# Optimization experiments

Measured on AMD Instinct MI355X. Metric: run time of the kernel, lower is better.

Reference implementation:

```python
import jax, jax.numpy as jnp
import numpy as np
import math

NUM_HEADS = 16
HEAD_SIZE = 64
HIDDEN = NUM_HEADS * HEAD_SIZE
LN_EPS = 1e-12


def setup_inputs() -> dict:
    key = jax.random.key(0)
    ks = jax.random.split(key, 8)
    B, Lw, Le, H = 8, 512, 64, HIDDEN
    scale = 0.02
    return {
        "word_hidden_states": jax.random.normal(ks[0], (B, Lw, H), jnp.float32),
        "entity_hidden_states": jax.random.normal(ks[1], (B, Le, H), jnp.float32),
        "attention_mask": jnp.zeros((B, 1, 1, Lw + Le), jnp.float32),
        "Wq": jax.random.normal(ks[2], (H, H), jnp.float32) * scale,
        "bq": jnp.zeros((H,), jnp.float32),
        "Wk": jax.random.normal(ks[3], (H, H), jnp.float32) * scale,
        "bk": jnp.zeros((H,), jnp.float32),
        "Wv": jax.random.normal(ks[4], (H, H), jnp.float32) * scale,
        "bv": jnp.zeros((H,), jnp.float32),
        "Wo": jax.random.normal(ks[5], (H, H), jnp.float32) * scale,
        "bo": jnp.zeros((H,), jnp.float32),
        "ln_w": jnp.ones((H,), jnp.float32),
        "ln_b": jnp.zeros((H,), jnp.float32),
    }


def _layernorm(x, w, b):
    u = jnp.mean(x, axis=-1, keepdims=True)
    s = jnp.mean(jnp.square(x - u), axis=-1, keepdims=True)
    return w * ((x - u) / jnp.sqrt(s + LN_EPS)) + b


def reference(word_hidden_states, entity_hidden_states, attention_mask,
              Wq, bq, Wk, bk, Wv, bv, Wo, bo, ln_w, ln_b):
    B, Lw, H = word_hidden_states.shape
    x = jnp.concatenate([word_hidden_states, entity_hidden_states], axis=1)  # [B,S,H]
    S = x.shape[1]

    def heads(t):  # [B,S,H] -> [B,nh,S,hd]
        return t.reshape(B, S, NUM_HEADS, HEAD_SIZE).transpose(0, 2, 1, 3)

    q = heads(x @ Wq + bq)
    k = heads(x @ Wk + bk)
    v = heads(x @ Wv + bv)

    scores = jnp.einsum("bhqd,bhkd->bhqk", q, k) / math.sqrt(HEAD_SIZE)
    scores = scores + attention_mask  # additive mask, broadcast [B,1,1,S]
    probs = jax.nn.softmax(scores, axis=-1)
    ctx = jnp.einsum("bhqk,bhkd->bhqd", probs, v)
    ctx = ctx.transpose(0, 2, 1, 3).reshape(B, S, H)

    # SelfOutput (shared weights) applied per-stream; equivalent on concat since
    # residual is the concatenated input and LayerNorm is per-token.
    out = _layernorm(ctx @ Wo + bo + x, ln_w, ln_b)
    return out[:, :Lw, :], out[:, Lw:, :]
```

## Files before the change

### kernel.cpp

```cpp
#include <hip/hip_runtime.h>

#define NHEADS 16
#define HDIM   64
#define HID    1024
#define BATCH  8
#define LW     512
#define LE     64
#define SEQ    576
#define MTOT   (BATCH * SEQ)

typedef unsigned short u16;
typedef __bf16 bf16x8 __attribute__((ext_vector_type(8)));
typedef float  f32x4  __attribute__((ext_vector_type(4)));

__device__ __forceinline__ u16 f2bf(float f) {
  union { float f; unsigned int i; } x;
  x.f = f;
  unsigned int u = x.i;
  unsigned int r = (u + 0x7FFFu + ((u >> 16) & 1u)) >> 16;
  return (u16)r;
}
__device__ __forceinline__ unsigned int pk2(float a, float b) {
  return (unsigned int)f2bf(a) | ((unsigned int)f2bf(b) << 16);
}

__device__ __forceinline__ void gload16(const u16* g, u16* l) {
  __builtin_amdgcn_global_load_lds(
      (const __attribute__((address_space(1))) void*)g,
      (__attribute__((address_space(3))) void*)l, 16, 0, 0);
}

__global__ __launch_bounds__(256) void prep_k(
    const float* __restrict__ w0, const float* __restrict__ w1,
    const float* __restrict__ w2, const float* __restrict__ w3,
    u16* __restrict__ wt,
    const float* __restrict__ word, const float* __restrict__ ent,
    u16* __restrict__ xb)
{
  const int bid = blockIdx.x, tid = threadIdx.x;
  if (bid < 4096) {
    __shared__ u16 tile[32][33];
    const int z = bid >> 10, rem = bid & 1023;
    const int bx = rem & 31, by = rem >> 5;
    const float* src = (z == 0) ? w0 : (z == 1) ? w1 : (z == 2) ? w2 : w3;
    u16* dst = wt + (size_t)z * HID * HID;
    const int tx = tid & 31, ty = tid >> 5;
    const int nx = bx * 32, ky = by * 32;
#pragma unroll
    for (int j = 0; j < 4; ++j)
      tile[ty * 4 + j][tx] = f2bf(src[(size_t)(ky + ty * 4 + j) * HID + nx + tx]);
    __syncthreads();
#pragma unroll
    for (int j = 0; j < 4; ++j)
      dst[(size_t)(nx + ty * 4 + j) * HID + ky + tx] = tile[tx][ty * 4 + j];
  } else {
    const int row = bid - 4096;
    const int bb = row / SEQ, ss = row - bb * SEQ;
    const float* src = (ss < LW) ? word + (size_t)(bb * LW + ss) * HID
                                 : ent  + (size_t)(bb * LE + (ss - LW)) * HID;
    float4 v = *(const float4*)(src + tid * 4);
    ushort4 o;
    o.x = f2bf(v.x); o.y = f2bf(v.y); o.z = f2bf(v.z); o.w = f2bf(v.w);
    *(ushort4*)(xb + (size_t)row * HID + tid * 4) = o;
  }
}

__global__ __launch_bounds__(256) void qkv_gemm_k(
    const u16* __restrict__ xb, const u16* __restrict__ wt,
    const float* __restrict__ bq, const float* __restrict__ bk, const float* __restrict__ bv,
    u16* __restrict__ q_ws, u16* __restrict__ k_ws, u16* __restrict__ v_ws)
{
  __shared__ u16 sh[4 * 64 * 68];
  const int which = blockIdx.z;
  const u16* W = wt + (size_t)which * HID * HID;
  const float* bias = (which == 0) ? bq : (which == 1) ? bk : bv;
  const int m0 = blockIdx.x * 128, n0 = blockIdx.y * 128;
  const int tid = threadIdx.x, lane = tid & 63, wv = tid >> 6;
  const int lr = lane & 15, quad = lane >> 4;
  const int wm = (wv >> 1) * 64, wn = (wv & 1) * 64;

  const int subrow = lane >> 3;
  const int gsw = ((lane & 7) ^ subrow) * 8;
  const int fsw = lr & 7;

  u16* As = sh;
  u16* Bs = sh + 8192;

  const f32x4 fz = {0.f, 0.f, 0.f, 0.f};
  f32x4 acc[4][4];
#pragma unroll
  for (int a = 0; a < 4; ++a)
#pragma unroll
    for (int b = 0; b < 4; ++b) acc[a][b] = fz;

  for (int ki = 0; ki < 16; ++ki) {
    const int k0 = ki * 64;
#pragma unroll
    for (int j = 0; j < 4; ++j) {
      int row = (wv * 4 + j) * 8 + subrow;
      u16* ldst = sh + ((wv * 4 + j) * 64 + lane) * 8;
      gload16(xb + (size_t)(m0 + row) * HID + k0 + gsw, ldst);
      gload16(W  + (size_t)(n0 + row) * HID + k0 + gsw, ldst + 8192);
    }
    __syncthreads();
#pragma unroll
    for (int ks = 0; ks < 2; ++ks) {
      bf16x8 af[4], bfr[4];
#pragma unroll
      for (int i = 0; i < 4; ++i) {
        af[i]  = *(const bf16x8*)(&As[(wm + i * 16 + lr) * 64 + (((ks * 4 + quad) ^ fsw) * 8)]);
        bfr[i] = *(const bf16x8*)(&Bs[(wn + i * 16 + lr) * 64 + (((ks * 4 + quad) ^ fsw) * 8)]);
      }
      if (which < 2) {
#pragma unroll
        for (int a = 0; a < 4; ++a)
#pragma unroll
          for (int b = 0; b < 4; ++b)
            acc[a][b] = __builtin_amdgcn_mfma_f32_16x16x32_bf16(bfr[a], af[b], acc[a][b], 0, 0, 0);
      } else {
#pragma unroll
        for (int a = 0; a < 4; ++a)
#pragma unroll
          for (int b = 0; b < 4; ++b)
            acc[a][b] = __builtin_amdgcn_mfma_f32_16x16x32_bf16(af[a], bfr[b], acc[a][b], 0, 0, 0);
      }
    }
    __syncthreads();
  }

  u16* tb = sh + wv * (64 * 68);
  const int head = (n0 + wn) >> 6;
  const int mbase = m0 + wm;
  const int bb = mbase / SEQ;
  const int ssb = mbase - bb * SEQ;

  if (which < 2) {
    float4 bias4[4];
#pragma unroll
    for (int ni = 0; ni < 4; ++ni)
      bias4[ni] = *(const float4*)(bias + n0 + wn + ni * 16 + quad * 4);
#pragma unroll
    for (int mi = 0; mi < 4; ++mi)
#pragma unroll
      for (int ni = 0; ni < 4; ++ni) {
        uint2 w2v;
        w2v.x = pk2(acc[ni][mi][0] + bias4[ni].x, acc[ni][mi][1] + bias4[ni].y);
        w2v.y = pk2(acc[ni][mi][2] + bias4[ni].z, acc[ni][mi][3] + bias4[ni].w);
        *(uint2*)(&tb[(mi * 16 + lr) * 68 + ni * 16 + quad * 4]) = w2v;
      }
    u16* drow = (which == 0 ? q_ws : k_ws)
              + ((size_t)(bb * NHEADS + head) * SEQ + ssb) * HDIM;
#pragma unroll
    for (int i = 0; i < 8; ++i) {
      int rrow = i * 8 + (lane >> 3);
      int seg = lane & 7;
      bf16x8 v8 = *(const bf16x8*)(&tb[rrow * 68 + seg * 8]);
      *(bf16x8*)(drow + (size_t)rrow * HDIM + seg * 8) = v8;
    }
  } else {
    float bcol[4];
#pragma unroll
    for (int ni = 0; ni < 4; ++ni) bcol[ni] = bias[n0 + wn + ni * 16 + lr];
#pragma unroll
    for (int mi = 0; mi < 4; ++mi)
#pragma unroll
      for (int ni = 0; ni < 4; ++ni) {
        uint2 w2v;
        w2v.x = pk2(acc[mi][ni][0] + bcol[ni], acc[mi][ni][1] + bcol[ni]);
        w2v.y = pk2(acc[mi][ni][2] + bcol[ni], acc[mi][ni][3] + bcol[ni]);
        *(uint2*)(&tb[(ni * 16 + lr) * 68 + (mi >> 1) * 32 + quad * 8 + (mi & 1) * 4]) = w2v;
      }
    u16* dcol = v_ws + ((size_t)(bb * NHEADS + head) * HDIM) * SEQ + ssb;
#pragma unroll
    for (int i = 0; i < 8; ++i) {
      int d = i * 8 + (lane >> 3);
      int seg = lane & 7;
      bf16x8 v8 = *(const bf16x8*)(&tb[d * 68 + seg * 8]);
      *(bf16x8*)(dcol + (size_t)d * SEQ + seg * 8) = v8;
    }
  }
}

__global__ __launch_bounds__(256) void attn_k(
    const u16* __restrict__ q_ws, const u16* __restrict__ k_ws,
    const u16* __restrict__ v_ws, const float* __restrict__ mask,
    u16* __restrict__ ctxh)
{
  __shared__ u16 Ks[4096];
  __shared__ u16 Vs[4096];
  __shared__ float ms[576];
  const int bhx = blockIdx.x, qt = blockIdx.y;
  const int b = bhx >> 4, h = bhx & 15;
  const int tid = threadIdx.x, lane = tid & 63, wv = tid >> 6;
  const int lr = lane & 15, quad = lane >> 4;
  const int q0 = qt * 64 + wv * 16;
  const u16* kbh = k_ws + (size_t)bhx * SEQ * HDIM;
  const u16* vbh = v_ws + (size_t)bhx * HDIM * SEQ;
  const u16* qp  = q_ws + ((size_t)bhx * SEQ + q0) * HDIM;
  const float* mrow = mask + b * SEQ;

  if (tid < 144) *(float4*)(&ms[tid * 4]) = *(const float4*)(mrow + tid * 4);

  const int subrow = lane >> 3;
  const int gsw = (lane & 7) ^ subrow;

  bf16x8 qf[2];
  qf[0] = *(const bf16x8*)(qp + lr * HDIM + quad * 8);
  qf[1] = *(const bf16x8*)(qp + lr * HDIM + 32 + quad * 8);

  const f32x4 fz = {0.f, 0.f, 0.f, 0.f};
  f32x4 oa[4] = {fz, fz, fz, fz};
  f32x4 rsv = fz;
  const int fA = lr & 7;

  for (int ci = 0; ci < 9; ++ci) {
    const int c = ci * 64;
#pragma unroll
    for (int j = 0; j < 2; ++j) {
      int row = (wv * 2 + j) * 8 + subrow;
      gload16(kbh + ((size_t)(c + row)) * HDIM + gsw * 8,
              &Ks[((wv * 2 + j) * 64 + lane) * 8]);
      gload16(vbh + (size_t)row * SEQ + c + gsw * 8,
              &Vs[((wv * 2 + j) * 64 + lane) * 8]);
    }
    __syncthreads();
    f32x4 s[4] = {fz, fz, fz, fz};
#pragma unroll
    for (int ks = 0; ks < 2; ++ks)
#pragma unroll
      for (int t = 0; t < 4; ++t) {
        bf16x8 kf = *(const bf16x8*)(&Ks[(t * 16 + lr) * 64 + (((ks * 4 + quad) ^ fA) * 8)]);
        s[t] = __builtin_amdgcn_mfma_f32_16x16x32_bf16(kf, qf[ks], s[t], 0, 0, 0);
      }
    unsigned int pk0[4], pk1[4];
#pragma unroll
    for (int t = 0; t < 4; ++t) {
      float4 mv = *(const float4*)(&ms[c + t * 16 + quad * 4]);
      s[t][0] = __expf(s[t][0] * 0.125f + mv.x);
      s[t][1] = __expf(s[t][1] * 0.125f + mv.y);
      s[t][2] = __expf(s[t][2] * 0.125f + mv.z);
      s[t][3] = __expf(s[t][3] * 0.125f + mv.w);
      rsv += s[t];
      pk0[t] = pk2(s[t][0], s[t][1]);
      pk1[t] = pk2(s[t][2], s[t][3]);
    }
#pragma unroll
    for (int ks = 0; ks < 2; ++ks) {
      union { unsigned int u[4]; bf16x8 v; } ap;
      ap.u[0] = pk0[ks * 2];     ap.u[1] = pk1[ks * 2];
      ap.u[2] = pk0[ks * 2 + 1]; ap.u[3] = pk1[ks * 2 + 1];
#pragma unroll
      for (int n = 0; n < 4; ++n) {
        bf16x8 vf = *(const bf16x8*)(&Vs[(n * 16 + lr) * 64 + (((ks * 4 + quad) ^ fA) * 8)]);
        oa[n] = __builtin_amdgcn_mfma_f32_16x16x32_bf16(ap.v, vf, oa[n], 0, 0, 0);
      }
    }
    __syncthreads();
  }

  float rl = rsv[0] + rsv[1] + rsv[2] + rsv[3];
  rl += __shfl_xor(rl, 16);
  rl += __shfl_xor(rl, 32);
  float inv = 1.0f / rl;
  float invr[4];
#pragma unroll
  for (int r = 0; r < 4; ++r) invr[r] = __shfl(inv, quad * 4 + r);

  u16* pw = (wv < 2) ? &Ks[wv * 2048] : &Vs[(wv - 2) * 2048];
#pragma unroll
  for (int n = 0; n < 4; ++n)
#pragma unroll
    for (int r = 0; r < 4; ++r)
      pw[(quad * 4 + r) * 68 + n * 16 + lr] = f2bf(oa[n][r] * invr[r]);
  const int token0 = b * SEQ + q0;
  u16* cb = ctxh + ((size_t)h * MTOT + token0) * HDIM;
#pragma unroll
  for (int i = 0; i < 2; ++i) {
    int row = lane & 15;
    int seg = (lane >> 4) + i * 4;
    bf16x8 v8 = *(const bf16x8*)(&pw[row * 68 + seg * 8]);
    *(bf16x8*)(cb + (size_t)row * HDIM + seg * 8) = v8;
  }
}

__global__ __launch_bounds__(256) void out_gemm_k(
    const u16* __restrict__ ctxh, const u16* __restrict__ wto,
    const float* __restrict__ bo,
    const float* __restrict__ word, const float* __restrict__ ent,
    float* __restrict__ y)
{
  __shared__ u16 sh[10240];
  u16* As = sh;
  u16* Bs = sh + 2048;
  const int m0 = blockIdx.x * 32, n0 = blockIdx.y * 128;
  const int tid = threadIdx.x, lane = tid & 63, wv = tid >> 6;
  const int lr = lane & 15, quad = lane >> 4;
  const int wn = wv * 32;
  const int subrow = lane >> 3;
  const int gsw = ((lane & 7) ^ subrow) * 8;
  const int fsw = lr & 7;

  const f32x4 fz = {0.f, 0.f, 0.f, 0.f};
  f32x4 acc[2][2];
#pragma unroll
  for (int mi = 0; mi < 2; ++mi)
#pragma unroll
    for (int ni = 0; ni < 2; ++ni) acc[mi][ni] = fz;

  for (int hb = 0; hb < 16; ++hb) {
    {
      int row = wv * 8 + subrow;
      gload16(ctxh + ((size_t)hb * MTOT + (m0 + row)) * HDIM + gsw,
              As + (wv * 64 + lane) * 8);
    }
#pragma unroll
    for (int j = 0; j < 4; ++j) {
      int row = (wv * 4 + j) * 8 + subrow;
      gload16(wto + (size_t)(n0 + row) * HID + hb * 64 + gsw,
              Bs + ((wv * 4 + j) * 64 + lane) * 8);
    }
    __syncthreads();
#pragma unroll
    for (int ks = 0; ks < 2; ++ks) {
      const int kc = (((ks * 4 + quad) ^ fsw) * 8);
      bf16x8 af[2], bfr[2];
#pragma unroll
      for (int i = 0; i < 2; ++i) {
        af[i]  = *(const bf16x8*)(&As[(i * 16 + lr) * 64 + kc]);
        bfr[i] = *(const bf16x8*)(&Bs[(wn + i * 16 + lr) * 64 + kc]);
      }
#pragma unroll
      for (int mi = 0; mi < 2; ++mi)
#pragma unroll
        for (int ni = 0; ni < 2; ++ni)
          acc[mi][ni] = __builtin_amdgcn_mfma_f32_16x16x32_bf16(af[mi], bfr[ni], acc[mi][ni], 0, 0, 0);
    }
    __syncthreads();
  }

#pragma unroll
  for (int mi = 0; mi < 2; ++mi) {
    int rowb = m0 + mi * 16 + quad * 4;
#pragma unroll
    for (int r = 0; r < 4; ++r) {
      int row = rowb + r;
      int bb = row / SEQ, ss = row - bb * SEQ;
      const float* res = (ss < LW) ? (word + (size_t)(bb * LW + ss) * HID)
                                   : (ent  + (size_t)(bb * LE + (ss - LW)) * HID);
#pragma unroll
      for (int ni = 0; ni < 2; ++ni) {
        int col = n0 + wn + ni * 16 + lr;
        y[(size_t)row * HID + col] = acc[mi][ni][r] + bo[col] + res[col];
      }
    }
  }
}

__global__ __launch_bounds__(256) void ln_k(
    const float* __restrict__ y, const float* __restrict__ lnw,
    const float* __restrict__ lnb, float* __restrict__ out)
{
  const int row = blockIdx.x;
  const int tid = threadIdx.x;
  __shared__ float ssum[4], sqq[4];

  const float* yr = y + (size_t)row * HID;
  float4 v = *(const float4*)(yr + tid * 4);
  float s = v.x + v.y + v.z + v.w;
  float q = v.x * v.x + v.y * v.y + v.z * v.z + v.w * v.w;
#pragma unroll
  for (int o = 32; o > 0; o >>= 1) { s += __shfl_xor(s, o); q += __shfl_xor(q, o); }
  if ((tid & 63) == 0) { ssum[tid >> 6] = s; sqq[tid >> 6] = q; }
  __syncthreads();
  s = ssum[0] + ssum[1] + ssum[2] + ssum[3];
  q = sqq[0] + sqq[1] + sqq[2] + sqq[3];
  float mean = s * (1.0f / HID);
  float var  = q * (1.0f / HID) - mean * mean;
  float rstd = rsqrtf(var + 1e-12f);

  int bb = row / SEQ, ss2 = row - bb * SEQ;
  float* dst = (ss2 < LW)
             ? out + (size_t)(bb * LW + ss2) * HID
             : out + (size_t)BATCH * LW * HID + (size_t)(bb * LE + (ss2 - LW)) * HID;

  float4 w4 = *(const float4*)(lnw + tid * 4);
  float4 b4 = *(const float4*)(lnb + tid * 4);
  float4 o4;
  o4.x = w4.x * (v.x - mean) * rstd + b4.x;
  o4.y = w4.y * (v.y - mean) * rstd + b4.y;
  o4.z = w4.z * (v.z - mean) * rstd + b4.z;
  o4.w = w4.w * (v.w - mean) * rstd + b4.w;
  *(float4*)(dst + tid * 4) = o4;
}

extern "C" void kernel_launch(void* const* d_in, const int* in_sizes, int n_in,
                              void* d_out, int out_size, void* d_ws, size_t ws_size,
                              hipStream_t stream) {
  const float* word = (const float*)d_in[0];
  const float* ent  = (const float*)d_in[1];
  const float* mask = (const float*)d_in[2];
  const float* Wq   = (const float*)d_in[3];
  const float* bq   = (const float*)d_in[4];
  const float* Wk   = (const float*)d_in[5];
  const float* bk   = (const float*)d_in[6];
  const float* Wv   = (const float*)d_in[7];
  const float* bv   = (const float*)d_in[8];
  const float* Wo   = (const float*)d_in[9];
  const float* bo   = (const float*)d_in[10];
  const float* lnw  = (const float*)d_in[11];
  const float* lnb  = (const float*)d_in[12];

  char* base = (char*)d_ws;
  u16*   wt   = (u16*)base;
  u16*   q_ws = (u16*)(base + (size_t)8 * 1024 * 1024);
  u16*   k_ws = q_ws + (size_t)MTOT * HID;
  u16*   v_ws = k_ws + (size_t)MTOT * HID;
  u16*   ctxh = v_ws + (size_t)MTOT * HID;
  char*  xy   = (char*)(ctxh + (size_t)MTOT * HID);
  u16*   xb   = (u16*)xy;
  float* y    = (float*)xy;

  hipLaunchKernelGGL(prep_k, dim3(4096 + MTOT), dim3(256), 0, stream,
                     Wq, Wk, Wv, Wo, wt, word, ent, xb);
  hipLaunchKernelGGL(qkv_gemm_k, dim3(MTOT / 128, HID / 128, 3), dim3(256), 0, stream,
                     xb, wt, bq, bk, bv, q_ws, k_ws, v_ws);
  hipLaunchKernelGGL(attn_k, dim3(BATCH * NHEADS, SEQ / 64), dim3(256), 0, stream,
                     q_ws, k_ws, v_ws, mask, ctxh);
  hipLaunchKernelGGL(out_gemm_k, dim3(MTOT / 32, HID / 128), dim3(256), 0, stream,
                     ctxh, wt + (size_t)3 * HID * HID, bo, word, ent, y);
  hipLaunchKernelGGL(ln_k, dim3(MTOT), dim3(256), 0, stream,
                     y, lnw, lnb, (float*)d_out);
}
```

Baseline: 197.2 us.

## Rewrite QKV GEMM as 256x256 tile, 8-wave, double-buffered pipelined kernel

```diff
diff --git a/kernel.cpp b/kernel.cpp
--- a/kernel.cpp
+++ b/kernel.cpp
@@ -65,118 +65,263 @@
   }
 }
 
-__global__ __launch_bounds__(256) void qkv_gemm_k(
+__device__ __forceinline__ void qkv_kstep(
+    u16* sh, const u16* asrc, const u16* bsrc, const int s, const int bo,
+    const bool g1, const bool g2, const bool vlast, const int which,
+    const int wm, const int wn, const int lr, const int quad, const int fsw,
+    const int tid, f32x4 (&acc)[8][4])
+{
+  u16* As = sh + bo;
+  u16* Bs = sh + bo + 16384;
+  const int obo = 32768 - bo;
+  bf16x8 afa[4][2], afb[4][2], bfr[4][2];
+
+#pragma unroll
+  for (int mi = 0; mi < 4; ++mi)
+#pragma unroll
+    for (int ks = 0; ks < 2; ++ks)
+      afa[mi][ks] = *(const bf16x8*)(&As[(wm + mi * 16 + lr) * 64 + (((ks * 4 + quad) ^ fsw) * 8)]);
+#pragma unroll
+  for (int ni = 0; ni < 2; ++ni)
+#pragma unroll
+    for (int ks = 0; ks < 2; ++ks)
+      bfr[ni][ks] = *(const bf16x8*)(&Bs[(wn + ni * 16 + lr) * 64 + (((ks * 4 + quad) ^ fsw) * 8)]);
+  if (g1) {
+    gload16(bsrc + (size_t)2 * 64 * HID + (s + 1) * 64, sh + obo + 16384 + 2 * 4096 + tid * 8);
+    gload16(bsrc + (size_t)3 * 64 * HID + (s + 1) * 64, sh + obo + 16384 + 3 * 4096 + tid * 8);
+  }
+  asm volatile("s_waitcnt lgkmcnt(8)" ::: "memory");
+  __builtin_amdgcn_s_barrier();
+  asm volatile("s_waitcnt lgkmcnt(0)" ::: "memory");
+  __builtin_amdgcn_sched_barrier(0);
+  __builtin_amdgcn_s_setprio(1);
+  if (which < 2) {
+#pragma unroll
+    for (int mi = 0; mi < 4; ++mi)
+#pragma unroll
+      for (int ni = 0; ni < 2; ++ni)
+#pragma unroll
+        for (int ks = 0; ks < 2; ++ks)
+          acc[mi][ni] = __builtin_amdgcn_mfma_f32_16x16x32_bf16(bfr[ni][ks], afa[mi][ks], acc[mi][ni], 0, 0, 0);
+  } else {
+#pragma unroll
+    for (int mi = 0; mi < 4; ++mi)
+#pragma unroll
+      for (int ni = 0; ni < 2; ++ni)
+#pragma unroll
+        for (int ks = 0; ks < 2; ++ks)
+          acc[mi][ni] = __builtin_amdgcn_mfma_f32_16x16x32_bf16(afa[mi][ks], bfr[ni][ks], acc[mi][ni], 0, 0, 0);
+  }
+  __builtin_amdgcn_s_setprio(0);
+  __builtin_amdgcn_s_barrier();
+
+#pragma unroll
+  for (int ni = 2; ni < 4; ++ni)
+#pragma unroll
+    for (int ks = 0; ks < 2; ++ks)
+      bfr[ni][ks] = *(const bf16x8*)(&Bs[(wn + ni * 16 + lr) * 64 + (((ks * 4 + quad) ^ fsw) * 8)]);
+  if (g2) {
+    gload16(asrc + (size_t)0 * 64 * HID + (s + 2) * 64, sh + bo + 0 * 4096 + tid * 8);
+    gload16(asrc + (size_t)2 * 64 * HID + (s + 2) * 64, sh + bo + 2 * 4096 + tid * 8);
+  }
+  __builtin_amdgcn_s_barrier();
+  asm volatile("s_waitcnt lgkmcnt(0)" ::: "memory");
+  __builtin_amdgcn_sched_barrier(0);
+  __builtin_amdgcn_s_setprio(1);
+  if (which < 2) {
+#pragma unroll
+    for (int mi = 0; mi < 4; ++mi)
+#pragma unroll
+      for (int ni = 2; ni < 4; ++ni)
+#pragma unroll
+        for (int ks = 0; ks < 2; ++ks)
+          acc[mi][ni] = __builtin_amdgcn_mfma_f32_16x16x32_bf16(bfr[ni][ks], afa[mi][ks], acc[mi][ni], 0, 0, 0);
+  } else {
+#pragma unroll
+    for (int mi = 0; mi < 4; ++mi)
+#pragma unroll
+      for (int ni = 2; ni < 4; ++ni)
+#pragma unroll
+        for (int ks = 0; ks < 2; ++ks)
+          acc[mi][ni] = __builtin_amdgcn_mfma_f32_16x16x32_bf16(afa[mi][ks], bfr[ni][ks], acc[mi][ni], 0, 0, 0);
+  }
+  __builtin_amdgcn_s_setprio(0);
+  __builtin_amdgcn_s_barrier();
+
+#pragma unroll
+  for (int mi = 0; mi < 4; ++mi)
+#pragma unroll
+    for (int ks = 0; ks < 2; ++ks)
+      afb[mi][ks] = *(const bf16x8*)(&As[(wm + 64 + mi * 16 + lr) * 64 + (((ks * 4 + quad) ^ fsw) * 8)]);
+  if (g2) {
+    gload16(bsrc + (size_t)0 * 64 * HID + (s + 2) * 64, sh + bo + 16384 + 0 * 4096 + tid * 8);
+    gload16(bsrc + (size_t)1 * 64 * HID + (s + 2) * 64, sh + bo + 16384 + 1 * 4096 + tid * 8);
+  }
+  __builtin_amdgcn_s_barrier();
+  asm volatile("s_waitcnt lgkmcnt(0)" ::: "memory");
+  __builtin_amdgcn_sched_barrier(0);
+  __builtin_amdgcn_s_setprio(1);
+  if (which < 2) {
+#pragma unroll
+    for (int mi = 0; mi < 4; ++mi)
+#pragma unroll
+      for (int ni = 0; ni < 2; ++ni)
+#pragma unroll
+        for (int ks = 0; ks < 2; ++ks)
+          acc[4 + mi][ni] = __builtin_amdgcn_mfma_f32_16x16x32_bf16(bfr[ni][ks], afb[mi][ks], acc[4 + mi][ni], 0, 0, 0);
+  } else {
+#pragma unroll
+    for (int mi = 0; mi < 4; ++mi)
+#pragma unroll
+      for (int ni = 0; ni < 2; ++ni)
+#pragma unroll
+        for (int ks = 0; ks < 2; ++ks)
+          acc[4 + mi][ni] = __builtin_amdgcn_mfma_f32_16x16x32_bf16(afb[mi][ks], bfr[ni][ks], acc[4 + mi][ni], 0, 0, 0);
+  }
+  __builtin_amdgcn_s_setprio(0);
+  __builtin_amdgcn_s_barrier();
+
+  if (g2) {
+    gload16(asrc + (size_t)1 * 64 * HID + (s + 2) * 64, sh + bo + 1 * 4096 + tid * 8);
+    gload16(asrc + (size_t)3 * 64 * HID + (s + 2) * 64, sh + bo + 3 * 4096 + tid * 8);
+  }
+  __builtin_amdgcn_s_barrier();
+  __builtin_amdgcn_sched_barrier(0);
+  __builtin_amdgcn_s_setprio(1);
+  if (which < 2) {
+#pragma unroll
+    for (int mi = 0; mi < 4; ++mi)
+#pragma unroll
+      for (int ni = 2; ni < 4; ++ni)
+#pragma unroll
+        for (int ks = 0; ks < 2; ++ks)
+          acc[4 + mi][ni] = __builtin_amdgcn_mfma_f32_16x16x32_bf16(bfr[ni][ks], afb[mi][ks], acc[4 + mi][ni], 0, 0, 0);
+  } else {
+#pragma unroll
+    for (int mi = 0; mi < 4; ++mi)
+#pragma unroll
+      for (int ni = 2; ni < 4; ++ni)
+#pragma unroll
+        for (int ks = 0; ks < 2; ++ks)
+          acc[4 + mi][ni] = __builtin_amdgcn_mfma_f32_16x16x32_bf16(afb[mi][ks], bfr[ni][ks], acc[4 + mi][ni], 0, 0, 0);
+  }
+  __builtin_amdgcn_s_setprio(0);
+  if (!vlast) asm volatile("s_waitcnt vmcnt(6)" ::: "memory");
+  else        asm volatile("s_waitcnt vmcnt(0)" ::: "memory");
+  __builtin_amdgcn_s_barrier();
+}
+
+__global__ __launch_bounds__(512, 2) void qkv_gemm_k(
     const u16* __restrict__ xb, const u16* __restrict__ wt,
     const float* __restrict__ bq, const float* __restrict__ bk, const float* __restrict__ bv,
     u16* __restrict__ q_ws, u16* __restrict__ k_ws, u16* __restrict__ v_ws)
 {
-  __shared__ u16 sh[4 * 64 * 68];
+  __shared__ u16 sh[65536];
   const int which = blockIdx.z;
   const u16* W = wt + (size_t)which * HID * HID;
   const float* bias = (which == 0) ? bq : (which == 1) ? bk : bv;
-  const int m0 = blockIdx.x * 128, n0 = blockIdx.y * 128;
+  const int m0 = blockIdx.x * 256, n0 = blockIdx.y * 256;
   const int tid = threadIdx.x, lane = tid & 63, wv = tid >> 6;
   const int lr = lane & 15, quad = lane >> 4;
-  const int wm = (wv >> 1) * 64, wn = (wv & 1) * 64;
-
-  const int subrow = lane >> 3;
-  const int gsw = ((lane & 7) ^ subrow) * 8;
+  const int wm = (wv >> 2) * 128, wn = (wv & 3) * 64;
   const int fsw = lr & 7;
 
-  u16* As = sh;
-  u16* Bs = sh + 8192;
+  const int srow = tid >> 3;
+  const int goff = ((tid & 7) ^ (srow & 7)) * 8;
+  const u16* asrc = xb + (size_t)(m0 + srow) * HID + goff;
+  const u16* bsrc = W  + (size_t)(n0 + srow) * HID + goff;
+
+  gload16(asrc + (size_t)0 * 64 * HID, sh + 0 * 4096 + tid * 8);
+  gload16(asrc + (size_t)1 * 64 * HID, sh + 1 * 4096 + tid * 8);
+  gload16(asrc + (size_t)2 * 64 * HID, sh + 2 * 4096 + tid * 8);
+  gload16(asrc + (size_t)3 * 64 * HID, sh + 3 * 4096 + tid * 8);
+  gload16(bsrc + (size_t)0 * 64 * HID, sh + 16384 + 0 * 4096 + tid * 8);
+  gload16(bsrc + (size_t)1 * 64 * HID, sh + 16384 + 1 * 4096 + tid * 8);
+  gload16(bsrc + (size_t)2 * 64 * HID, sh + 16384 + 2 * 4096 + tid * 8);
+  gload16(bsrc + (size_t)3 * 64 * HID, sh + 16384 + 3 * 4096 + tid * 8);
+  gload16(asrc + (size_t)0 * 64 * HID + 64, sh + 32768 + 0 * 4096 + tid * 8);
+  gload16(asrc + (size_t)2 * 64 * HID + 64, sh + 32768 + 2 * 4096 + tid * 8);
+  gload16(bsrc + (size_t)0 * 64 * HID + 64, sh + 32768 + 16384 + 0 * 4096 + tid * 8);
+  gload16(bsrc + (size_t)1 * 64 * HID + 64, sh + 32768 + 16384 + 1 * 4096 + tid * 8);
+  gload16(asrc + (size_t)1 * 64 * HID + 64, sh + 32768 + 1 * 4096 + tid * 8);
+  gload16(asrc + (size_t)3 * 64 * HID + 64, sh + 32768 + 3 * 4096 + tid * 8);
+  asm volatile("s_waitcnt vmcnt(6)" ::: "memory");
+  __builtin_amdgcn_s_barrier();
 
   const f32x4 fz = {0.f, 0.f, 0.f, 0.f};
-  f32x4 acc[4][4];
-#pragma unroll
-  for (int a = 0; a < 4; ++a)
+  f32x4 acc[8][4];
+#pragma unroll
+  for (int a = 0; a < 8; ++a)
 #pragma unroll
     for (int b = 0; b < 4; ++b) acc[a][b] = fz;
 
-  for (int ki = 0; ki < 16; ++ki) {
-    const int k0 = ki * 64;
-#pragma unroll
-    for (int j = 0; j < 4; ++j) {
-      int row = (wv * 4 + j) * 8 + subrow;
-      u16* ldst = sh + ((wv * 4 + j) * 64 + lane) * 8;
-      gload16(xb + (size_t)(m0 + row) * HID + k0 + gsw, ldst);
-      gload16(W  + (size_t)(n0 + row) * HID + k0 + gsw, ldst + 8192);
-    }
-    __syncthreads();
-#pragma unroll
-    for (int ks = 0; ks < 2; ++ks) {
-      bf16x8 af[4], bfr[4];
-#pragma unroll
-      for (int i = 0; i < 4; ++i) {
-        af[i]  = *(const bf16x8*)(&As[(wm + i * 16 + lr) * 64 + (((ks * 4 + quad) ^ fsw) * 8)]);
-        bfr[i] = *(const bf16x8*)(&Bs[(wn + i * 16 + lr) * 64 + (((ks * 4 + quad) ^ fsw) * 8)]);
-      }
-      if (which < 2) {
-#pragma unroll
-        for (int a = 0; a < 4; ++a)
-#pragma unroll
-          for (int b = 0; b < 4; ++b)
-            acc[a][b] = __builtin_amdgcn_mfma_f32_16x16x32_bf16(bfr[a], af[b], acc[a][b], 0, 0, 0);
-      } else {
-#pragma unroll
-        for (int a = 0; a < 4; ++a)
-#pragma unroll
-          for (int b = 0; b < 4; ++b)
-            acc[a][b] = __builtin_amdgcn_mfma_f32_16x16x32_bf16(af[a], bfr[b], acc[a][b], 0, 0, 0);
-      }
-    }
-    __syncthreads();
+  for (int s = 0; s < 16; s += 2) {
+    qkv_kstep(sh, asrc, bsrc, s,     0,     true,   s < 14, s >= 14, which,
+              wm, wn, lr, quad, fsw, tid, acc);
+    qkv_kstep(sh, asrc, bsrc, s + 1, 32768, s < 14, s < 13, s >= 13, which,
+              wm, wn, lr, quad, fsw, tid, acc);
   }
 
   u16* tb = sh + wv * (64 * 68);
   const int head = (n0 + wn) >> 6;
-  const int mbase = m0 + wm;
-  const int bb = mbase / SEQ;
-  const int ssb = mbase - bb * SEQ;
 
   if (which < 2) {
     float4 bias4[4];
 #pragma unroll
     for (int ni = 0; ni < 4; ++ni)
       bias4[ni] = *(const float4*)(bias + n0 + wn + ni * 16 + quad * 4);
-#pragma unroll
-    for (int mi = 0; mi < 4; ++mi)
-#pragma unroll
-      for (int ni = 0; ni < 4; ++ni) {
-        uint2 w2v;
-        w2v.x = pk2(acc[ni][mi][0] + bias4[ni].x, acc[ni][mi][1] + bias4[ni].y);
-        w2v.y = pk2(acc[ni][mi][2] + bias4[ni].z, acc[ni][mi][3] + bias4[ni].w);
-        *(uint2*)(&tb[(mi * 16 + lr) * 68 + ni * 16 + quad * 4]) = w2v;
+    u16* qk = (which == 0 ? q_ws : k_ws);
+#pragma unroll
+    for (int g = 0; g < 2; ++g) {
+      const int mbase = m0 + wm + g * 64;
+      const int bb = mbase / SEQ;
+      const int ssb = mbase - bb * SEQ;
+#pragma unroll
+      for (int mi = 0; mi < 4; ++mi)
+#pragma unroll
+        for (int ni = 0; ni < 4; ++ni) {
+          const f32x4 a = acc[g * 4 + mi][ni];
+          uint2 w2v;
+          w2v.x = pk2(a[0] + bias4[ni].x, a[1] + bias4[ni].y);
+          w2v.y = pk2(a[2] + bias4[ni].z, a[3] + bias4[ni].w);
+          *(uint2*)(&tb[(mi * 16 + lr) * 68 + ni * 16 + quad * 4]) = w2v;
+        }
+      u16* drow = qk + ((size_t)(bb * NHEADS + head) * SEQ + ssb) * HDIM;
+#pragma unroll
+      for (int i = 0; i < 8; ++i) {
+        int rrow = i * 8 + (lane >> 3);
+        int seg = lane & 7;
+        bf16x8 v8 = *(const bf16x8*)(&tb[rrow * 68 + seg * 8]);
+        *(bf16x8*)(drow + (size_t)rrow * HDIM + seg * 8) = v8;
       }
-    u16* drow = (which == 0 ? q_ws : k_ws)
-              + ((size_t)(bb * NHEADS + head) * SEQ + ssb) * HDIM;
-#pragma unroll
-    for (int i = 0; i < 8; ++i) {
-      int rrow = i * 8 + (lane >> 3);
-      int seg = lane & 7;
-      bf16x8 v8 = *(const bf16x8*)(&tb[rrow * 68 + seg * 8]);
-      *(bf16x8*)(drow + (size_t)rrow * HDIM + seg * 8) = v8;
     }
   } else {
     float bcol[4];
 #pragma unroll
     for (int ni = 0; ni < 4; ++ni) bcol[ni] = bias[n0 + wn + ni * 16 + lr];
 #pragma unroll
-    for (int mi = 0; mi < 4; ++mi)
-#pragma unroll
-      for (int ni = 0; ni < 4; ++ni) {
-        uint2 w2v;
-        w2v.x = pk2(acc[mi][ni][0] + bcol[ni], acc[mi][ni][1] + bcol[ni]);
-        w2v.y = pk2(acc[mi][ni][2] + bcol[ni], acc[mi][ni][3] + bcol[ni]);
-        *(uint2*)(&tb[(ni * 16 + lr) * 68 + (mi >> 1) * 32 + quad * 8 + (mi & 1) * 4]) = w2v;
+    for (int g = 0; g < 2; ++g) {
+      const int mbase = m0 + wm + g * 64;
+      const int bb = mbase / SEQ;
+      const int ssb = mbase - bb * SEQ;
+#pragma unroll
+      for (int mi = 0; mi < 4; ++mi)
+#pragma unroll
+        for (int ni = 0; ni < 4; ++ni) {
+          const f32x4 a = acc[g * 4 + mi][ni];
+          uint2 w2v;
+          w2v.x = pk2(a[0] + bcol[ni], a[1] + bcol[ni]);
+          w2v.y = pk2(a[2] + bcol[ni], a[3] + bcol[ni]);
+          *(uint2*)(&tb[(ni * 16 + lr) * 68 + (mi >> 1) * 32 + quad * 8 + (mi & 1) * 4]) = w2v;
+        }
+      u16* dcol = v_ws + ((size_t)(bb * NHEADS + head) * HDIM) * SEQ + ssb;
+#pragma unroll
+      for (int i = 0; i < 8; ++i) {
+        int d = i * 8 + (lane >> 3);
+        int seg = lane & 7;
+        bf16x8 v8 = *(const bf16x8*)(&tb[d * 68 + seg * 8]);
+        *(bf16x8*)(dcol + (size_t)d * SEQ + seg * 8) = v8;
       }
-    u16* dcol = v_ws + ((size_t)(bb * NHEADS + head) * HDIM) * SEQ + ssb;
-#pragma unroll
-    for (int i = 0; i < 8; ++i) {
-      int d = i * 8 + (lane >> 3);
-      int seg = lane & 7;
-      bf16x8 v8 = *(const bf16x8*)(&tb[d * 68 + seg * 8]);
-      *(bf16x8*)(dcol + (size_t)d * SEQ + seg * 8) = v8;
     }
   }
 }
@@ -422,7 +567,7 @@
 
   hipLaunchKernelGGL(prep_k, dim3(4096 + MTOT), dim3(256), 0, stream,
                      Wq, Wk, Wv, Wo, wt, word, ent, xb);
-  hipLaunchKernelGGL(qkv_gemm_k, dim3(MTOT / 128, HID / 128, 3), dim3(256), 0, stream,
+  hipLaunchKernelGGL(qkv_gemm_k, dim3(MTOT / 256, HID / 256, 3), dim3(512), 0, stream,
                      xb, wt, bq, bk, bv, q_ws, k_ws, v_ws);
   hipLaunchKernelGGL(attn_k, dim3(BATCH * NHEADS, SEQ / 64), dim3(256), 0, stream,
                      q_ws, k_ws, v_ws, mask, ctxh);
```

Result: slower. 232.3 us (+17.8%).

## Double-buffer QKV GEMM with 256x128 tiles, 8 waves, and split-phase prefetch

Applied to the files above, without the earlier changes.

```diff
diff --git a/kernel.cpp b/kernel.cpp
--- a/kernel.cpp
+++ b/kernel.cpp
@@ -65,26 +65,39 @@
   }
 }
 
-__global__ __launch_bounds__(256) void qkv_gemm_k(
+__global__ __launch_bounds__(512, 2) void qkv_gemm_k(
     const u16* __restrict__ xb, const u16* __restrict__ wt,
     const float* __restrict__ bq, const float* __restrict__ bk, const float* __restrict__ bv,
     u16* __restrict__ q_ws, u16* __restrict__ k_ws, u16* __restrict__ v_ws)
 {
-  __shared__ u16 sh[4 * 64 * 68];
+  __shared__ u16 sh[49152];
   const int which = blockIdx.z;
   const u16* W = wt + (size_t)which * HID * HID;
   const float* bias = (which == 0) ? bq : (which == 1) ? bk : bv;
-  const int m0 = blockIdx.x * 128, n0 = blockIdx.y * 128;
+  const int m0 = blockIdx.x * 256, n0 = blockIdx.y * 128;
   const int tid = threadIdx.x, lane = tid & 63, wv = tid >> 6;
   const int lr = lane & 15, quad = lane >> 4;
   const int wm = (wv >> 1) * 64, wn = (wv & 1) * 64;
-
-  const int subrow = lane >> 3;
-  const int gsw = ((lane & 7) ^ subrow) * 8;
   const int fsw = lr & 7;
 
-  u16* As = sh;
-  u16* Bs = sh + 8192;
+  const int srow = tid >> 3;
+  const int goff = ((tid & 7) ^ (srow & 7)) * 8;
+  const u16* asrc = xb + (size_t)(m0 + srow) * HID + goff;
+  const u16* bsrc = W  + (size_t)(n0 + srow) * HID + goff;
+  const int ldst = tid * 8;
+
+  gload16(asrc + (size_t)0 * 64 * HID, sh + 0 * 4096 + ldst);
+  gload16(asrc + (size_t)1 * 64 * HID, sh + 1 * 4096 + ldst);
+  gload16(asrc + (size_t)2 * 64 * HID, sh + 2 * 4096 + ldst);
+  gload16(asrc + (size_t)3 * 64 * HID, sh + 3 * 4096 + ldst);
+  gload16(bsrc + (size_t)0 * 64 * HID, sh + 16384 + 0 * 4096 + ldst);
+  gload16(bsrc + (size_t)1 * 64 * HID, sh + 16384 + 1 * 4096 + ldst);
+  gload16(asrc + (size_t)0 * 64 * HID + 64, sh + 24576 + 0 * 4096 + ldst);
+  gload16(asrc + (size_t)1 * 64 * HID + 64, sh + 24576 + 1 * 4096 + ldst);
+  gload16(asrc + (size_t)2 * 64 * HID + 64, sh + 24576 + 2 * 4096 + ldst);
+  gload16(asrc + (size_t)3 * 64 * HID + 64, sh + 24576 + 3 * 4096 + ldst);
+  asm volatile("s_waitcnt vmcnt(4)" ::: "memory");
+  __builtin_amdgcn_s_barrier();
 
   const f32x4 fz = {0.f, 0.f, 0.f, 0.f};
   f32x4 acc[4][4];
@@ -93,39 +106,88 @@
 #pragma unroll
     for (int b = 0; b < 4; ++b) acc[a][b] = fz;
 
-  for (int ki = 0; ki < 16; ++ki) {
-    const int k0 = ki * 64;
-#pragma unroll
-    for (int j = 0; j < 4; ++j) {
-      int row = (wv * 4 + j) * 8 + subrow;
-      u16* ldst = sh + ((wv * 4 + j) * 64 + lane) * 8;
-      gload16(xb + (size_t)(m0 + row) * HID + k0 + gsw, ldst);
-      gload16(W  + (size_t)(n0 + row) * HID + k0 + gsw, ldst + 8192);
-    }
-    __syncthreads();
-#pragma unroll
-    for (int ks = 0; ks < 2; ++ks) {
-      bf16x8 af[4], bfr[4];
-#pragma unroll
-      for (int i = 0; i < 4; ++i) {
-        af[i]  = *(const bf16x8*)(&As[(wm + i * 16 + lr) * 64 + (((ks * 4 + quad) ^ fsw) * 8)]);
-        bfr[i] = *(const bf16x8*)(&Bs[(wn + i * 16 + lr) * 64 + (((ks * 4 + quad) ^ fsw) * 8)]);
-      }
-      if (which < 2) {
-#pragma unroll
-        for (int a = 0; a < 4; ++a)
-#pragma unroll
-          for (int b = 0; b < 4; ++b)
-            acc[a][b] = __builtin_amdgcn_mfma_f32_16x16x32_bf16(bfr[a], af[b], acc[a][b], 0, 0, 0);
-      } else {
-#pragma unroll
-        for (int a = 0; a < 4; ++a)
-#pragma unroll
-          for (int b = 0; b < 4; ++b)
-            acc[a][b] = __builtin_amdgcn_mfma_f32_16x16x32_bf16(af[a], bfr[b], acc[a][b], 0, 0, 0);
-      }
-    }
-    __syncthreads();
+  for (int s = 0; s < 16; ++s) {
+    const int bo  = (s & 1) * 24576;
+    const int obo = 24576 - bo;
+    u16* As = sh + bo;
+    u16* Bs = sh + bo + 16384;
+
+    bf16x8 afr[4][2], bfr[4][2];
+#pragma unroll
+    for (int mi = 0; mi < 4; ++mi)
+#pragma unroll
+      for (int ks = 0; ks < 2; ++ks)
+        afr[mi][ks] = *(const bf16x8*)(&As[(wm + mi * 16 + lr) * 64 + (((ks * 4 + quad) ^ fsw) * 8)]);
+#pragma unroll
+    for (int ni = 0; ni < 2; ++ni)
+#pragma unroll
+      for (int ks = 0; ks < 2; ++ks)
+        bfr[ni][ks] = *(const bf16x8*)(&Bs[(wn + ni * 16 + lr) * 64 + (((ks * 4 + quad) ^ fsw) * 8)]);
+    if (s < 15) {
+      gload16(bsrc + (size_t)0 * 64 * HID + (s + 1) * 64, sh + obo + 16384 + 0 * 4096 + ldst);
+      gload16(bsrc + (size_t)1 * 64 * HID + (s + 1) * 64, sh + obo + 16384 + 1 * 4096 + ldst);
+    }
+    asm volatile("s_waitcnt lgkmcnt(8)" ::: "memory");
+    __builtin_amdgcn_s_barrier();
+    asm volatile("s_waitcnt lgkmcnt(0)" ::: "memory");
+    __builtin_amdgcn_sched_barrier(0);
+    __builtin_amdgcn_s_setprio(1);
+    if (which < 2) {
+#pragma unroll
+      for (int mi = 0; mi < 4; ++mi)
+#pragma unroll
+        for (int ni = 0; ni < 2; ++ni)
+#pragma unroll
+          for (int ks = 0; ks < 2; ++ks)
+            acc[ni][mi] = __builtin_amdgcn_mfma_f32_16x16x32_bf16(bfr[ni][ks], afr[mi][ks], acc[ni][mi], 0, 0, 0);
+    } else {
+#pragma unroll
+      for (int mi = 0; mi < 4; ++mi)
+#pragma unroll
+        for (int ni = 0; ni < 2; ++ni)
+#pragma unroll
+          for (int ks = 0; ks < 2; ++ks)
+            acc[mi][ni] = __builtin_amdgcn_mfma_f32_16x16x32_bf16(afr[mi][ks], bfr[ni][ks], acc[mi][ni], 0, 0, 0);
+    }
+    __builtin_amdgcn_s_setprio(0);
+    __builtin_amdgcn_s_barrier();
+
+#pragma unroll
+    for (int ni = 2; ni < 4; ++ni)
+#pragma unroll
+      for (int ks = 0; ks < 2; ++ks)
+        bfr[ni][ks] = *(const bf16x8*)(&Bs[(wn + ni * 16 + lr) * 64 + (((ks * 4 + quad) ^ fsw) * 8)]);
+    if (s < 14) {
+      gload16(asrc + (size_t)0 * 64 * HID + (s + 2) * 64, sh + bo + 0 * 4096 + ldst);
+      gload16(asrc + (size_t)1 * 64 * HID + (s + 2) * 64, sh + bo + 1 * 4096 + ldst);
+      gload16(asrc + (size_t)2 * 64 * HID + (s + 2) * 64, sh + bo + 2 * 4096 + ldst);
+      gload16(asrc + (size_t)3 * 64 * HID + (s + 2) * 64, sh + bo + 3 * 4096 + ldst);
+    }
+    __builtin_amdgcn_s_barrier();
+    asm volatile("s_waitcnt lgkmcnt(0)" ::: "memory");
+    __builtin_amdgcn_sched_barrier(0);
+    __builtin_amdgcn_s_setprio(1);
+    if (which < 2) {
+#pragma unroll
+      for (int mi = 0; mi < 4; ++mi)
+#pragma unroll
+        for (int ni = 2; ni < 4; ++ni)
+#pragma unroll
+          for (int ks = 0; ks < 2; ++ks)
+            acc[ni][mi] = __builtin_amdgcn_mfma_f32_16x16x32_bf16(bfr[ni][ks], afr[mi][ks], acc[ni][mi], 0, 0, 0);
+    } else {
+#pragma unroll
+      for (int mi = 0; mi < 4; ++mi)
+#pragma unroll
+        for (int ni = 2; ni < 4; ++ni)
+#pragma unroll
+          for (int ks = 0; ks < 2; ++ks)
+            acc[mi][ni] = __builtin_amdgcn_mfma_f32_16x16x32_bf16(afr[mi][ks], bfr[ni][ks], acc[mi][ni], 0, 0, 0);
+    }
+    __builtin_amdgcn_s_setprio(0);
+    if (s < 14) asm volatile("s_waitcnt vmcnt(4)" ::: "memory");
+    else        asm volatile("s_waitcnt vmcnt(0)" ::: "memory");
+    __builtin_amdgcn_s_barrier();
   }
 
   u16* tb = sh + wv * (64 * 68);
@@ -422,7 +484,7 @@
 
   hipLaunchKernelGGL(prep_k, dim3(4096 + MTOT), dim3(256), 0, stream,
                      Wq, Wk, Wv, Wo, wt, word, ent, xb);
-  hipLaunchKernelGGL(qkv_gemm_k, dim3(MTOT / 128, HID / 128, 3), dim3(256), 0, stream,
+  hipLaunchKernelGGL(qkv_gemm_k, dim3(MTOT / 256, HID / 128, 3), dim3(512), 0, stream,
                      xb, wt, bq, bk, bv, q_ws, k_ws, v_ws);
   hipLaunchKernelGGL(attn_k, dim3(BATCH * NHEADS, SEQ / 64), dim3(256), 0, stream,
                      q_ws, k_ws, v_ws, mask, ctxh);
```

Result: no change. 200.9 us (+1.9%).

## Rewrite QKV GEMM with 256x256 tiles and double-buffered ping-pong pipeline

Applied to the files above, without the earlier changes.

```diff
diff --git a/kernel.cpp b/kernel.cpp
--- a/kernel.cpp
+++ b/kernel.cpp
@@ -65,118 +65,213 @@
   }
 }
 
-__global__ __launch_bounds__(256) void qkv_gemm_k(
+#define Q_MFMA(AF, BF, H, NB)                                                 \
+  if (which < 2) {                                                            \
+    _Pragma("unroll")                                                         \
+    for (int mi = 0; mi < 4; ++mi)                                            \
+      _Pragma("unroll")                                                       \
+      for (int nj = 0; nj < 2; ++nj)                                          \
+        _Pragma("unroll")                                                     \
+        for (int ks = 0; ks < 2; ++ks)                                        \
+          acc[(H)*4 + (NB) + nj][mi] = __builtin_amdgcn_mfma_f32_16x16x32_bf16( \
+              BF[nj][ks], AF[mi][ks], acc[(H)*4 + (NB) + nj][mi], 0, 0, 0);   \
+  } else {                                                                    \
+    _Pragma("unroll")                                                         \
+    for (int mi = 0; mi < 4; ++mi)                                            \
+      _Pragma("unroll")                                                       \
+      for (int nj = 0; nj < 2; ++nj)                                          \
+        _Pragma("unroll")                                                     \
+        for (int ks = 0; ks < 2; ++ks)                                        \
+          acc[(H)*4 + mi][(NB) + nj] = __builtin_amdgcn_mfma_f32_16x16x32_bf16( \
+              AF[mi][ks], BF[nj][ks], acc[(H)*4 + mi][(NB) + nj], 0, 0, 0);   \
+  }
+
+__global__ __launch_bounds__(512, 2) void qkv_gemm_k(
     const u16* __restrict__ xb, const u16* __restrict__ wt,
     const float* __restrict__ bq, const float* __restrict__ bk, const float* __restrict__ bv,
     u16* __restrict__ q_ws, u16* __restrict__ k_ws, u16* __restrict__ v_ws)
 {
-  __shared__ u16 sh[4 * 64 * 68];
+  __shared__ u16 sh[65536];
   const int which = blockIdx.z;
   const u16* W = wt + (size_t)which * HID * HID;
   const float* bias = (which == 0) ? bq : (which == 1) ? bk : bv;
-  const int m0 = blockIdx.x * 128, n0 = blockIdx.y * 128;
+  const int m0 = blockIdx.x * 256, n0 = blockIdx.y * 256;
   const int tid = threadIdx.x, lane = tid & 63, wv = tid >> 6;
   const int lr = lane & 15, quad = lane >> 4;
-  const int wm = (wv >> 1) * 64, wn = (wv & 1) * 64;
-
-  const int subrow = lane >> 3;
-  const int gsw = ((lane & 7) ^ subrow) * 8;
+  const int wm = (wv >> 2) * 128, wn = (wv & 3) * 64;
   const int fsw = lr & 7;
-
-  u16* As = sh;
-  u16* Bs = sh + 8192;
+  const int k0o = ((quad ^ fsw)) * 8;
+  const int k1o = (((4 + quad) ^ fsw)) * 8;
+  const int aCh = (wv >> 2) * 8192;
+  const int bCh = (wv & 3) * 4096;
+  const int arow = lr * 64;
+
+  const int srow = tid >> 3;
+  const int goff = ((tid & 7) ^ (srow & 7)) * 8;
+  const u16* asrc = xb + (size_t)(m0 + srow) * HID + goff;
+  const u16* bsrc = W  + (size_t)(n0 + srow) * HID + goff;
+  const int ldst = tid * 8;
+
+#pragma unroll
+  for (int c = 0; c < 4; ++c)
+    gload16(asrc + (size_t)c * 64 * HID, sh + c * 4096 + ldst);
+#pragma unroll
+  for (int c = 0; c < 4; ++c)
+    gload16(bsrc + (size_t)c * 64 * HID, sh + 16384 + c * 4096 + ldst);
+#pragma unroll
+  for (int c = 0; c < 4; ++c)
+    gload16(asrc + (size_t)c * 64 * HID + 64, sh + 32768 + c * 4096 + ldst);
+#pragma unroll
+  for (int c = 0; c < 4; ++c)
+    gload16(bsrc + (size_t)c * 64 * HID + 64, sh + 32768 + 16384 + c * 4096 + ldst);
+  asm volatile("s_waitcnt vmcnt(8)" ::: "memory");
+  __builtin_amdgcn_s_barrier();
 
   const f32x4 fz = {0.f, 0.f, 0.f, 0.f};
-  f32x4 acc[4][4];
-#pragma unroll
-  for (int a = 0; a < 4; ++a)
+  f32x4 acc[8][4];
+#pragma unroll
+  for (int a = 0; a < 8; ++a)
 #pragma unroll
     for (int b = 0; b < 4; ++b) acc[a][b] = fz;
 
-  for (int ki = 0; ki < 16; ++ki) {
-    const int k0 = ki * 64;
-#pragma unroll
-    for (int j = 0; j < 4; ++j) {
-      int row = (wv * 4 + j) * 8 + subrow;
-      u16* ldst = sh + ((wv * 4 + j) * 64 + lane) * 8;
-      gload16(xb + (size_t)(m0 + row) * HID + k0 + gsw, ldst);
-      gload16(W  + (size_t)(n0 + row) * HID + k0 + gsw, ldst + 8192);
-    }
-    __syncthreads();
-#pragma unroll
-    for (int ks = 0; ks < 2; ++ks) {
-      bf16x8 af[4], bfr[4];
-#pragma unroll
-      for (int i = 0; i < 4; ++i) {
-        af[i]  = *(const bf16x8*)(&As[(wm + i * 16 + lr) * 64 + (((ks * 4 + quad) ^ fsw) * 8)]);
-        bfr[i] = *(const bf16x8*)(&Bs[(wn + i * 16 + lr) * 64 + (((ks * 4 + quad) ^ fsw) * 8)]);
-      }
-      if (which < 2) {
-#pragma unroll
-        for (int a = 0; a < 4; ++a)
-#pragma unroll
-          for (int b = 0; b < 4; ++b)
-            acc[a][b] = __builtin_amdgcn_mfma_f32_16x16x32_bf16(bfr[a], af[b], acc[a][b], 0, 0, 0);
-      } else {
-#pragma unroll
-        for (int a = 0; a < 4; ++a)
-#pragma unroll
-          for (int b = 0; b < 4; ++b)
-            acc[a][b] = __builtin_amdgcn_mfma_f32_16x16x32_bf16(af[a], bfr[b], acc[a][b], 0, 0, 0);
-      }
-    }
-    __syncthreads();
+  for (int s = 0; s < 16; ++s) {
+    const int bo = (s & 1) << 15;
+    u16* As = sh + bo;
+    u16* Bs = sh + bo + 16384;
+    const int sOff = (s + 2) * 64;
+    const bool gpre = (s < 14);
+
+    bf16x8 af[4][2], bfL[2][2], bfH[2][2];
+
+#pragma unroll
+    for (int mi = 0; mi < 4; ++mi) {
+      af[mi][0] = *(const bf16x8*)(&As[aCh + mi * 1024 + arow + k0o]);
+      af[mi][1] = *(const bf16x8*)(&As[aCh + mi * 1024 + arow + k1o]);
+    }
+#pragma unroll
+    for (int nj = 0; nj < 2; ++nj) {
+      bfL[nj][0] = *(const bf16x8*)(&Bs[bCh + nj * 1024 + arow + k0o]);
+      bfL[nj][1] = *(const bf16x8*)(&Bs[bCh + nj * 1024 + arow + k1o]);
+    }
+    asm volatile("s_waitcnt lgkmcnt(8)" ::: "memory");
+    __builtin_amdgcn_s_barrier();
+    asm volatile("s_waitcnt lgkmcnt(0)" ::: "memory");
+    __builtin_amdgcn_sched_barrier(0);
+    __builtin_amdgcn_s_setprio(1);
+    Q_MFMA(af, bfL, 0, 0)
+    __builtin_amdgcn_s_setprio(0);
+    __builtin_amdgcn_s_barrier();
+
+#pragma unroll
+    for (int nj = 0; nj < 2; ++nj) {
+      bfH[nj][0] = *(const bf16x8*)(&Bs[bCh + (2 + nj) * 1024 + arow + k0o]);
+      bfH[nj][1] = *(const bf16x8*)(&Bs[bCh + (2 + nj) * 1024 + arow + k1o]);
+    }
+    if (gpre) {
+      gload16(asrc + (size_t)0 * 64 * HID + sOff, sh + bo + 0 * 4096 + ldst);
+      gload16(asrc + (size_t)2 * 64 * HID + sOff, sh + bo + 2 * 4096 + ldst);
+    }
+    __builtin_amdgcn_s_barrier();
+    asm volatile("s_waitcnt lgkmcnt(0)" ::: "memory");
+    __builtin_amdgcn_sched_barrier(0);
+    __builtin_amdgcn_s_setprio(1);
+    Q_MFMA(af, bfH, 0, 2)
+    __builtin_amdgcn_s_setprio(0);
+    __builtin_amdgcn_s_barrier();
+
+#pragma unroll
+    for (int mi = 0; mi < 4; ++mi) {
+      af[mi][0] = *(const bf16x8*)(&As[aCh + 4096 + mi * 1024 + arow + k0o]);
+      af[mi][1] = *(const bf16x8*)(&As[aCh + 4096 + mi * 1024 + arow + k1o]);
+    }
+    if (gpre) {
+      gload16(bsrc + (size_t)0 * 64 * HID + sOff, sh + bo + 16384 + 0 * 4096 + ldst);
+      gload16(bsrc + (size_t)1 * 64 * HID + sOff, sh + bo + 16384 + 1 * 4096 + ldst);
+      gload16(bsrc + (size_t)2 * 64 * HID + sOff, sh + bo + 16384 + 2 * 4096 + ldst);
+      gload16(bsrc + (size_t)3 * 64 * HID + sOff, sh + bo + 16384 + 3 * 4096 + ldst);
+    }
+    __builtin_amdgcn_s_barrier();
+    asm volatile("s_waitcnt lgkmcnt(0)" ::: "memory");
+    __builtin_amdgcn_sched_barrier(0);
+    __builtin_amdgcn_s_setprio(1);
+    Q_MFMA(af, bfH, 1, 2)
+    __builtin_amdgcn_s_setprio(0);
+    __builtin_amdgcn_s_barrier();
+
+    if (gpre) {
+      gload16(asrc + (size_t)1 * 64 * HID + sOff, sh + bo + 1 * 4096 + ldst);
+      gload16(asrc + (size_t)3 * 64 * HID + sOff, sh + bo + 3 * 4096 + ldst);
+    }
+    __builtin_amdgcn_s_barrier();
+    __builtin_amdgcn_sched_barrier(0);
+    __builtin_amdgcn_s_setprio(1);
+    Q_MFMA(af, bfL, 1, 0)
+    __builtin_amdgcn_s_setprio(0);
+    if (s < 14)       asm volatile("s_waitcnt vmcnt(8)" ::: "memory");
+    else if (s == 14) asm volatile("s_waitcnt vmcnt(0)" ::: "memory");
+    __builtin_amdgcn_s_barrier();
   }
 
   u16* tb = sh + wv * (64 * 68);
   const int head = (n0 + wn) >> 6;
-  const int mbase = m0 + wm;
-  const int bb = mbase / SEQ;
-  const int ssb = mbase - bb * SEQ;
 
   if (which < 2) {
     float4 bias4[4];
 #pragma unroll
     for (int ni = 0; ni < 4; ++ni)
       bias4[ni] = *(const float4*)(bias + n0 + wn + ni * 16 + quad * 4);
-#pragma unroll
-    for (int mi = 0; mi < 4; ++mi)
-#pragma unroll
-      for (int ni = 0; ni < 4; ++ni) {
-        uint2 w2v;
-        w2v.x = pk2(acc[ni][mi][0] + bias4[ni].x, acc[ni][mi][1] + bias4[ni].y);
-        w2v.y = pk2(acc[ni][mi][2] + bias4[ni].z, acc[ni][mi][3] + bias4[ni].w);
-        *(uint2*)(&tb[(mi * 16 + lr) * 68 + ni * 16 + quad * 4]) = w2v;
+    u16* qk = (which == 0 ? q_ws : k_ws);
+#pragma unroll
+    for (int g = 0; g < 2; ++g) {
+      const int mbase = m0 + wm + g * 64;
+      const int bb = mbase / SEQ;
+      const int ssb = mbase - bb * SEQ;
+#pragma unroll
+      for (int mi = 0; mi < 4; ++mi)
+#pragma unroll
+        for (int ni = 0; ni < 4; ++ni) {
+          const f32x4 a = acc[g * 4 + ni][mi];
+          uint2 w2v;
+          w2v.x = pk2(a[0] + bias4[ni].x, a[1] + bias4[ni].y);
+          w2v.y = pk2(a[2] + bias4[ni].z, a[3] + bias4[ni].w);
+          *(uint2*)(&tb[(mi * 16 + lr) * 68 + ni * 16 + quad * 4]) = w2v;
+        }
+      u16* drow = qk + ((size_t)(bb * NHEADS + head) * SEQ + ssb) * HDIM;
+#pragma unroll
+      for (int i = 0; i < 8; ++i) {
+        int rrow = i * 8 + (lane >> 3);
+        int seg = lane & 7;
+        bf16x8 v8 = *(const bf16x8*)(&tb[rrow * 68 + seg * 8]);
+        *(bf16x8*)(drow + (size_t)rrow * HDIM + seg * 8) = v8;
       }
-    u16* drow = (which == 0 ? q_ws : k_ws)
-              + ((size_t)(bb * NHEADS + head) * SEQ + ssb) * HDIM;
-#pragma unroll
-    for (int i = 0; i < 8; ++i) {
-      int rrow = i * 8 + (lane >> 3);
-      int seg = lane & 7;
-      bf16x8 v8 = *(const bf16x8*)(&tb[rrow * 68 + seg * 8]);
-      *(bf16x8*)(drow + (size_t)rrow * HDIM + seg * 8) = v8;
     }
   } else {
     float bcol[4];
 #pragma unroll
     for (int ni = 0; ni < 4; ++ni) bcol[ni] = bias[n0 + wn + ni * 16 + lr];
 #pragma unroll
-    for (int mi = 0; mi < 4; ++mi)
-#pragma unroll
-      for (int ni = 0; ni < 4; ++ni) {
-        uint2 w2v;
-        w2v.x = pk2(acc[mi][ni][0] + bcol[ni], acc[mi][ni][1] + bcol[ni]);
-        w2v.y = pk2(acc[mi][ni][2] + bcol[ni], acc[mi][ni][3] + bcol[ni]);
-        *(uint2*)(&tb[(ni * 16 + lr) * 68 + (mi >> 1) * 32 + quad * 8 + (mi & 1) * 4]) = w2v;
+    for (int g = 0; g < 2; ++g) {
+      const int mbase = m0 + wm + g * 64;
+      const int bb = mbase / SEQ;
+      const int ssb = mbase - bb * SEQ;
+#pragma unroll
+      for (int mi = 0; mi < 4; ++mi)
+#pragma unroll
+        for (int ni = 0; ni < 4; ++ni) {
+          const f32x4 a = acc[g * 4 + mi][ni];
+          uint2 w2v;
+          w2v.x = pk2(a[0] + bcol[ni], a[1] + bcol[ni]);
+          w2v.y = pk2(a[2] + bcol[ni], a[3] + bcol[ni]);
+          *(uint2*)(&tb[(ni * 16 + lr) * 68 + (mi >> 1) * 32 + quad * 8 + (mi & 1) * 4]) = w2v;
+        }
+      u16* dcol = v_ws + ((size_t)(bb * NHEADS + head) * HDIM) * SEQ + ssb;
+#pragma unroll
+      for (int i = 0; i < 8; ++i) {
+        int d = i * 8 + (lane >> 3);
+        int seg = lane & 7;
+        bf16x8 v8 = *(const bf16x8*)(&tb[d * 68 + seg * 8]);
+        *(bf16x8*)(dcol + (size_t)d * SEQ + seg * 8) = v8;
       }
-    u16* dcol = v_ws + ((size_t)(bb * NHEADS + head) * HDIM) * SEQ + ssb;
-#pragma unroll
-    for (int i = 0; i < 8; ++i) {
-      int d = i * 8 + (lane >> 3);
-      int seg = lane & 7;
-      bf16x8 v8 = *(const bf16x8*)(&tb[d * 68 + seg * 8]);
-      *(bf16x8*)(dcol + (size_t)d * SEQ + seg * 8) = v8;
     }
   }
 }
@@ -422,7 +517,7 @@
 
   hipLaunchKernelGGL(prep_k, dim3(4096 + MTOT), dim3(256), 0, stream,
                      Wq, Wk, Wv, Wo, wt, word, ent, xb);
-  hipLaunchKernelGGL(qkv_gemm_k, dim3(MTOT / 128, HID / 128, 3), dim3(256), 0, stream,
+  hipLaunchKernelGGL(qkv_gemm_k, dim3(MTOT / 256, HID / 256, 3), dim3(512), 0, stream,
                      xb, wt, bq, bk, bv, q_ws, k_ws, v_ws);
   hipLaunchKernelGGL(attn_k, dim3(BATCH * NHEADS, SEQ / 64), dim3(256), 0, stream,
                      q_ws, k_ws, v_ws, mask, ctxh);
```

Result: no change. 197.1 us (-0.1%).
